# Kernel optimization log

Hardware: AMD Instinct MI355X
Metric: run time of the kernel (lower is better)

The kernel has to match this reference:

```python
import jax, jax.numpy as jnp
import numpy as np

B = 16       # graphs per batch
N = 256      # nodes per graph (Hi-C submatrix bins)
NT = B * N   # total nodes
E = 131072   # total edges
DIN = 32     # input feature dim (HYPERPARAMETERS['input_shape'])
H1, H2 = 16, 32
HID = 32     # ContactCNN hidden dim
W7 = 7       # final conv width


def setup_inputs() -> dict:
    key = jax.random.key(0)
    ks = jax.random.split(key, 16)
    x = jax.random.normal(ks[0], (NT, DIN), dtype=jnp.float32)
    edge_index = jax.random.randint(ks[1], (2, E), 0, NT, dtype=jnp.int64)
    edge_attr = jax.random.uniform(ks[2], (E,), dtype=jnp.float32)
    batch_index = jnp.repeat(jnp.arange(B, dtype=jnp.int64), N)
    s = 0.1
    params = dict(
        W0=jax.random.normal(ks[3], (DIN, H1), dtype=jnp.float32) * s,
        b0=jnp.zeros((H1,), dtype=jnp.float32),
        W1=jax.random.normal(ks[4], (H1, H2), dtype=jnp.float32) * s,
        b1=jnp.zeros((H2,), dtype=jnp.float32),
        W2=jax.random.normal(ks[5], (H2, H2), dtype=jnp.float32) * s,
        b2=jnp.zeros((H2,), dtype=jnp.float32),
        Wc=jax.random.normal(ks[6], (HID, H2), dtype=jnp.float32) * s,  # 1x1 conv: [out=HID, in=H2]
        bc=jnp.zeros((HID,), dtype=jnp.float32),
        Wp=jax.random.normal(ks[7], (1, HID, W7, W7), dtype=jnp.float32) * s,  # OIHW
        bp=jnp.zeros((1,), dtype=jnp.float32),
    )
    return dict(x=x, edge_index=edge_index, edge_attr=edge_attr,
                batch_index=batch_index, **params)


def _gcn_norm(edge_index, edge_weight, n):
    # PyG gcn_norm with improved=True (self-loop fill value 2.0)
    src, dst = edge_index[0], edge_index[1]
    loop = jnp.arange(n, dtype=src.dtype)
    src_a = jnp.concatenate([src, loop])
    dst_a = jnp.concatenate([dst, loop])
    w_a = jnp.concatenate([edge_weight, jnp.full((n,), 2.0, dtype=edge_weight.dtype)])
    deg = jax.ops.segment_sum(w_a, dst_a, num_segments=n)
    deg_safe = jnp.where(deg > 0, deg, 1.0)
    dinv = jnp.where(deg > 0, jax.lax.rsqrt(deg_safe), 0.0)
    norm = dinv[src_a] * w_a * dinv[dst_a]
    return src_a, dst_a, norm


def _gcn_layer(h, W, b, src_a, dst_a, norm, n):
    h = h @ W                                  # [n, out]
    msg = norm[:, None] * h[src_a]             # gather + scale
    return jax.ops.segment_sum(msg, dst_a, num_segments=n) + b  # scatter-add


def reference(x, edge_index, edge_attr, batch_index,
              W0, b0, W1, b1, W2, b2, Wc, bc, Wp, bp):
    n = x.shape[0]
    src_a, dst_a, norm = _gcn_norm(edge_index, edge_attr, n)
    h = jax.nn.relu(_gcn_layer(x, W0, b0, src_a, dst_a, norm, n))
    h = jax.nn.relu(_gcn_layer(h, W1, b1, src_a, dst_a, norm, n))
    h = jax.nn.relu(_gcn_layer(h, W2, b2, src_a, dst_a, norm, n))
    z = h.reshape(B, N, -1)                    # process_graph_batch
    # ContactCNN: broadcast outer product -> 1x1 conv -> ReLU -> 7x7 conv -> sigmoid
    zm = jnp.einsum('bid,bjd->bdij', z, z)     # [B, D, N, N]
    c = jax.nn.relu(jnp.einsum('bdij,hd->bhij', zm, Wc) + bc[None, :, None, None])
    s = jax.lax.conv_general_dilated(
        c, Wp, window_strides=(1, 1), padding='SAME',
        dimension_numbers=('NCHW', 'OIHW', 'NCHW')) + bp[None, :, None, None]
    return jax.nn.sigmoid(s)                   # [B, 1, N, N]
```

## Files before the change

### kernel.cpp

```cpp
#include <hip/hip_runtime.h>
#include <hip/hip_bf16.h>
#include <hip/hip_fp16.h>

#define NT 4096
#define NE 131072

#define OFF_DEG  0
#define OFF_A    16384
#define OFF_G1T  33570816
#define OFF_G2T  33701888
#define OFF_G3T  33964032
#define OFF_H3   34226176
#define OFF_W2T  34488320

typedef __attribute__((ext_vector_type(8))) short bf16x8;
typedef __attribute__((ext_vector_type(4))) float f32x4;

__device__ inline unsigned int align16(unsigned int hi, unsigned int lo) {
#if __has_builtin(__builtin_amdgcn_alignbit)
    return __builtin_amdgcn_alignbit(hi, lo, 16);
#else
    return (lo >> 16) | (hi << 16);
#endif
}

__device__ inline unsigned short bfb(float x) {
    return __hip_bfloat16_raw(__float2bfloat16(x)).x;
}

__device__ inline void atomic_add_bf16(unsigned short* base, unsigned int idx, float v) {
    unsigned long long addr = (unsigned long long)(base + (idx & ~1u));
    unsigned int bits = ((unsigned int)bfb(v)) << ((idx & 1u) * 16);
    asm volatile("global_atomic_pk_add_bf16 %0, %1, off" :: "v"(addr), "v"(bits) : "memory");
}


__global__ __launch_bounds__(256) void k_zerodeg(const int* __restrict__ ei,
                                                 const float* __restrict__ ew,
                                                 float* __restrict__ deg,
                                                 unsigned short* __restrict__ A16) {
    int blk = blockIdx.x, tid = threadIdx.x;
    uint4 z4 = {0u, 0u, 0u, 0u};
    uint4* ap = (uint4*)(A16 + (size_t)blk * 16384);
    #pragma unroll
    for (int k = 0; k < 8; k++) ap[tid + k * 256] = z4;
    int gid = blk * 256 + tid;
    if (gid < NE) atomicAdd(&deg[ei[NE + gid]], ew[gid]);
}

__global__ void k_scatter(const int* __restrict__ ei, const float* __restrict__ ew,
                          const float* __restrict__ deg, unsigned short* __restrict__ A16,
                          const float* __restrict__ x, const float* __restrict__ W0,
                          unsigned short* __restrict__ G1T,
                          const float* __restrict__ Wp, unsigned int* __restrict__ w2) {
    int e = blockIdx.x * 256 + threadIdx.x;
    if (e < NE) {
        int s = ei[e], d = ei[NE + e];
        float v = rsqrtf(deg[s] + 2.f) * ew[e] * rsqrtf(deg[d] + 2.f);
        atomic_add_bf16(A16, (unsigned int)d * 4096u + (unsigned int)s, v);
    }
    if (e < NT) {
        atomic_add_bf16(A16, (unsigned int)e * 4097u, 2.f / (deg[e] + 2.f));
    }
    if (e < NT * 16) {
        int node = e & 4095, co = e >> 12;
        const float4* xr = (const float4*)(x + node * 32);
        float a = 0.f;
        #pragma unroll
        for (int r = 0; r < 8; r++) {
            float4 f = xr[r];
            a += f.x * W0[(r*4+0)*16 + co] + f.y * W0[(r*4+1)*16 + co]
               + f.z * W0[(r*4+2)*16 + co] + f.w * W0[(r*4+3)*16 + co];
        }
        G1T[co * 4096 + node] = bfb(a);
    }
    if (e >= NE - 1568) {
        int k = e - (NE - 1568);
        __half hh = __float2half(Wp[k]);
        __half2 h2 = __halves2half2(hh, hh);
        w2[k] = *(unsigned int*)&h2;
    }
}


template <int NIN, int NOUT, bool LAST>
__global__ __launch_bounds__(512) void k_gcn(const unsigned short* __restrict__ A16,
                                             const unsigned short* __restrict__ Gt,
                                             const float* __restrict__ bias,
                                             const float* __restrict__ W,
                                             unsigned short* __restrict__ Gout) {
    constexpr int T = NIN / 16;
    __shared__ float red[8][T][16][16];
    __shared__ unsigned short wtile[16 * 40];
    int mt = blockIdx.x;
    int tid = threadIdx.x;
    int w = tid >> 6, lane = tid & 63, m = lane & 15, q = lane >> 4;
    int kw = w * 512;

    const unsigned short* arow = A16 + (size_t)(mt * 16 + m) * 4096 + kw + q * 8;
    f32x4 acc[T];
    #pragma unroll
    for (int t = 0; t < T; t++) acc[t] = (f32x4){0.f, 0.f, 0.f, 0.f};

    bf16x8 wfrag;
    if (!LAST && w < NOUT / 16) {
        #pragma unroll
        for (int j = 0; j < 8; j++) {
            int ci = q * 8 + j;
            wfrag[j] = (ci < NIN) ? (short)bfb(W[ci * NOUT + w * 16 + m]) : (short)0;
        }
    }

    #pragma unroll 4
    for (int s = 0; s < 16; s++) {
        bf16x8 bA = *(const bf16x8*)(arow + s * 32);
        #pragma unroll
        for (int t = 0; t < T; t++) {
            bf16x8 af = *(const bf16x8*)(Gt + (size_t)(t * 16 + m) * 4096 + kw + q * 8 + s * 32);
            acc[t] = __builtin_amdgcn_mfma_f32_16x16x32_bf16(af, bA, acc[t], 0, 0, 0);
        }
    }
    #pragma unroll
    for (int t = 0; t < T; t++)
        #pragma unroll
        for (int r = 0; r < 4; r++) red[w][t][q*4 + r][m] = acc[t][r];
    __syncthreads();

    if (tid < T * 256) {
        int dstp = tid & 15, cop = (tid >> 4) & 15, t = tid >> 8;
        float sum = 0.f;
        #pragma unroll
        for (int w8 = 0; w8 < 8; w8++) sum += red[w8][t][cop][dstp];
        int co = t * 16 + cop;
        float val = fmaxf(sum + bias[co], 0.f);
        if (LAST) Gout[(size_t)(mt * 16 + dstp) * 32 + co] = bfb(val);
        else      wtile[dstp * 40 + co] = bfb(val);
    }
    if (!LAST && NIN == 16 && tid >= 256 && tid < 512) {
        int idx = tid - 256;
        wtile[(idx & 15) * 40 + 16 + ((idx >> 4) & 15)] = 0;
    }
    __syncthreads();

    if (!LAST && w < NOUT / 16) {
        bf16x8 af = *(const bf16x8*)&wtile[m * 40 + q * 8];
        f32x4 o = (f32x4){0.f, 0.f, 0.f, 0.f};
        o = __builtin_amdgcn_mfma_f32_16x16x32_bf16(af, wfrag, o, 0, 0, 0);
        uint2 ov;
        ov.x = (unsigned int)bfb(o[0]) | ((unsigned int)bfb(o[1]) << 16);
        ov.y = (unsigned int)bfb(o[2]) | ((unsigned int)bfb(o[3]) << 16);
        *(uint2*)&Gout[(size_t)(w * 16 + m) * 4096 + mt * 16 + q * 4] = ov;
    }
}


__global__ __launch_bounds__(512, 4) void k_cc(const unsigned short* __restrict__ h3,
                                               const float* __restrict__ Wc,
                                               const float* __restrict__ bc,
                                               const unsigned int* __restrict__ w2,
                                               const float* __restrict__ bp,
                                               float* __restrict__ out) {
    __shared__ unsigned short zs[256 * 40];
    __shared__ float wcs[32 * 36];
    __shared__ __align__(16) unsigned short ct[2 * 16 * 272];
    __shared__ __align__(16) unsigned short pt[2][2048];

    int band = blockIdx.x, bb = blockIdx.y;
    int i0 = band * 8;
    int tid = threadIdx.x;
    int lane = tid & 63, w = tid >> 6;
    int m = lane & 15, q = lane >> 4;

    {
        int row = tid >> 1, half = tid & 1;
        const uint4* src = (const uint4*)(h3 + (size_t)(bb * 256 + row) * 32) + half * 2;
        uint4 v0 = src[0], v1 = src[1];
        uint4* dst = (uint4*)&zs[row * 40 + half * 16];
        dst[0] = v0; dst[1] = v1;
    }
    #pragma unroll
    for (int k = tid; k < 1024; k += 512) wcs[(k >> 5) * 36 + (k & 31)] = Wc[k];
    for (int k = tid; k < 2 * 16 * 136; k += 512) ((unsigned int*)ct)[k] = 0;
    __syncthreads();

    bf16x8 bt;
    bool wok;
    {
        int r = i0 - 3 + m;
        wok = (unsigned)r < 256u;
        r = r < 0 ? 0 : (r > 255 ? 255 : r);
        bt = *(const bf16x8*)&zs[r * 40 + q * 8];
    }
    float zaf[2][8];
    #pragma unroll
    for (int jt2 = 0; jt2 < 2; jt2++) {
        bf16x8 za = *(const bf16x8*)&zs[((w * 2 + jt2) * 16 + m) * 40 + q * 8];
        #pragma unroll
        for (int e = 0; e < 8; e++)
            zaf[jt2][e] = __uint_as_float(((unsigned int)(unsigned short)za[e]) << 16);
    }

    int gg = tid >> 8, idx = tid & 255;
    int tx = idx & 31, ty = idx >> 5;
    __half2 acc[4];
    __half2 zh = __float2half2_rn(0.f);
    #pragma unroll
    for (int p = 0; p < 4; p++) acc[p] = zh;

    for (int it = 0; it < 16; it++) {
        #pragma unroll
        for (int g = 0; g < 2; g++) {
            int h = it * 2 + g;
            float wf[8];
            *(float4*)&wf[0] = *(const float4*)&wcs[h * 36 + q * 8];
            *(float4*)&wf[4] = *(const float4*)&wcs[h * 36 + q * 8 + 4];
            float bch = bc[h];
            #pragma unroll
            for (int jt2 = 0; jt2 < 2; jt2++) {
                bf16x8 afv;
                #pragma unroll
                for (int e = 0; e < 8; e++) afv[e] = (short)bfb(zaf[jt2][e] * wf[e]);
                int pos = 4 + (w * 2 + jt2) * 16 + q * 4;
                f32x4 d = (f32x4){0.f, 0.f, 0.f, 0.f};
                d = __builtin_amdgcn_mfma_f32_16x16x32_bf16(afv, bt, d, 0, 0, 0);
                if (wok) {
                    float v0 = fmaxf(d[0] + bch, 0.f);
                    float v1 = fmaxf(d[1] + bch, 0.f);
                    float v2 = fmaxf(d[2] + bch, 0.f);
                    float v3 = fmaxf(d[3] + bch, 0.f);
                    __half2 h0 = __floats2half2_rn(v0, v1);
                    __half2 h1 = __floats2half2_rn(v2, v3);
                    uint2 o2;
                    o2.x = *(unsigned int*)&h0;
                    o2.y = *(unsigned int*)&h1;
                    *(uint2*)&ct[g * 4352 + m * 272 + pos] = o2;
                }
            }
        }
        __syncthreads();

        {
            const unsigned short* C = ct + gg * 4352;
            const __half2* wrow = (const __half2*)w2 + (it * 2 + gg) * 49;
            #pragma unroll
            for (int dr = 0; dr < 7; dr++) {
                const uint4* p4 = (const uint4*)&C[(ty + dr) * 272 + tx * 8];
                uint4 ua = p4[0], ub = p4[1];
                unsigned int E[8] = {ua.x, ua.y, ua.z, ua.w, ub.x, ub.y, ub.z, ub.w};
                unsigned int O[7];
                #pragma unroll
                for (int k = 0; k < 7; k++) O[k] = align16(E[k + 1], E[k]);
                #pragma unroll
                for (int dj = 0; dj < 7; dj++) {
                    __half2 wv = wrow[dr * 7 + dj];
                    #pragma unroll
                    for (int pr = 0; pr < 4; pr++) {
                        int s = 2 * pr + dj + 1;
                        unsigned int pv = (s & 1) ? O[s >> 1] : E[s >> 1];
                        acc[pr] = __hfma2(wv, *(__half2*)&pv, acc[pr]);
                    }
                }
            }
        }
        __syncthreads();
    }

    {
        uint4 v;
        v.x = *(unsigned int*)&acc[0];
        v.y = *(unsigned int*)&acc[1];
        v.z = *(unsigned int*)&acc[2];
        v.w = *(unsigned int*)&acc[3];
        *(uint4*)&pt[gg][ty * 256 + tx * 8] = v;
    }
    __syncthreads();

    {
        int base = tid * 4;
        float fs[4];
        #pragma unroll
        for (int e = 0; e < 4; e++) fs[e] = 0.f;
        #pragma unroll
        for (int g = 0; g < 2; g++) {
            uint2 v = *(const uint2*)&pt[g][base];
            unsigned int uu[2] = {v.x, v.y};
            #pragma unroll
            for (int d = 0; d < 2; d++) {
                float2 f = __half22float2(*(__half2*)&uu[d]);
                fs[2 * d] += f.x; fs[2 * d + 1] += f.y;
            }
        }
        float bpv = bp[0];
        float4 r;
        r.x = 1.0f / (1.0f + __expf(-(fs[0] + bpv)));
        r.y = 1.0f / (1.0f + __expf(-(fs[1] + bpv)));
        r.z = 1.0f / (1.0f + __expf(-(fs[2] + bpv)));
        r.w = 1.0f / (1.0f + __expf(-(fs[3] + bpv)));
        int row = base >> 8, col = base & 255;
        *(float4*)&out[((size_t)(bb * 256) + i0 + row) * 256 + col] = r;
    }
}


extern "C" void kernel_launch(void* const* d_in, const int* in_sizes, int n_in,
                              void* d_out, int out_size, void* d_ws, size_t ws_size,
                              hipStream_t stream) {
    const float* x  = (const float*)d_in[0];
    const int*   ei = (const int*)d_in[1];
    const float* ew = (const float*)d_in[2];
    const float* W0 = (const float*)d_in[4];
    const float* b0 = (const float*)d_in[5];
    const float* W1 = (const float*)d_in[6];
    const float* b1 = (const float*)d_in[7];
    const float* W2 = (const float*)d_in[8];
    const float* b2 = (const float*)d_in[9];
    const float* Wc = (const float*)d_in[10];
    const float* bc = (const float*)d_in[11];
    const float* Wp = (const float*)d_in[12];
    const float* bp = (const float*)d_in[13];

    char* ws = (char*)d_ws;
    float*          deg  = (float*)(ws + OFF_DEG);
    unsigned short* A16  = (unsigned short*)(ws + OFF_A);
    unsigned short* G1T  = (unsigned short*)(ws + OFF_G1T);
    unsigned short* G2T  = (unsigned short*)(ws + OFF_G2T);
    unsigned short* G3T  = (unsigned short*)(ws + OFF_G3T);
    unsigned short* H3   = (unsigned short*)(ws + OFF_H3);
    unsigned int*   w2t  = (unsigned int*)(ws + OFF_W2T);

    (void)hipMemsetAsync(deg, 0, 16384, stream);

    k_zerodeg<<<1024, 256, 0, stream>>>(ei, ew, deg, A16);
    k_scatter<<<NE/256, 256, 0, stream>>>(ei, ew, deg, A16, x, W0, G1T, Wp, w2t);

    k_gcn<16, 32, false><<<256, 512, 0, stream>>>(A16, G1T, b0, W1, G2T);
    k_gcn<32, 32, false><<<256, 512, 0, stream>>>(A16, G2T, b1, W2, G3T);
    k_gcn<32, 32, true> <<<256, 512, 0, stream>>>(A16, G3T, b2, nullptr, H3);

    k_cc<<<dim3(32, 16), 512, 0, stream>>>(H3, Wc, bc, w2t, bp, (float*)d_out);
}
```

Before: 206.6 us.

## Enlarge contact-CNN row bands to 16 and prefetch adjacency fragments in GCN

The contact kernel now computes 16 output rows per block instead of 8, so each block produces a 22-row halo tile with two MFMA column tiles. This halves the redundant halo recomputation and removes the cross-group half-precision reduction through shared memory, since each thread now accumulates both channel groups itself. The 7x7 stencil loads are batched ahead of the FMAs. Separately, the GCN kernel preloads all 16 adjacency fragments into registers before the MFMA loop. In exchange, register pressure rises in both kernels, and the contact grid halves to 256 blocks, which may lower occupancy and parallelism.

```diff
diff --git a/kernel.cpp b/kernel.cpp
--- a/kernel.cpp
+++ b/kernel.cpp
@@ -98,6 +98,11 @@
     int kw = w * 512;
 
     const unsigned short* arow = A16 + (size_t)(mt * 16 + m) * 4096 + kw + q * 8;
+
+    bf16x8 bA[16];
+    #pragma unroll
+    for (int s = 0; s < 16; s++) bA[s] = *(const bf16x8*)(arow + s * 32);
+
     f32x4 acc[T];
     #pragma unroll
     for (int t = 0; t < T; t++) acc[t] = (f32x4){0.f, 0.f, 0.f, 0.f};
@@ -111,13 +116,13 @@
         }
     }
 
-    #pragma unroll 4
+    const unsigned short* gbase = Gt + kw + q * 8 + (size_t)m * 4096;
+    #pragma unroll
     for (int s = 0; s < 16; s++) {
-        bf16x8 bA = *(const bf16x8*)(arow + s * 32);
         #pragma unroll
         for (int t = 0; t < T; t++) {
-            bf16x8 af = *(const bf16x8*)(Gt + (size_t)(t * 16 + m) * 4096 + kw + q * 8 + s * 32);
-            acc[t] = __builtin_amdgcn_mfma_f32_16x16x32_bf16(af, bA, acc[t], 0, 0, 0);
+            bf16x8 af = *(const bf16x8*)(gbase + (size_t)t * 16 * 4096 + s * 32);
+            acc[t] = __builtin_amdgcn_mfma_f32_16x16x32_bf16(af, bA[s], acc[t], 0, 0, 0);
         }
     }
     #pragma unroll
@@ -154,22 +159,22 @@
 }
 
 
-__global__ __launch_bounds__(512, 4) void k_cc(const unsigned short* __restrict__ h3,
-                                               const float* __restrict__ Wc,
-                                               const float* __restrict__ bc,
-                                               const unsigned int* __restrict__ w2,
-                                               const float* __restrict__ bp,
-                                               float* __restrict__ out) {
-    __shared__ unsigned short zs[256 * 40];
+__global__ __launch_bounds__(512) void k_cc(const unsigned short* __restrict__ h3,
+                                            const float* __restrict__ Wc,
+                                            const float* __restrict__ bc,
+                                            const unsigned int* __restrict__ w2,
+                                            const float* __restrict__ bp,
+                                            float* __restrict__ out) {
+    __shared__ __align__(16) unsigned short pool[2 * 32 * 280];
     __shared__ float wcs[32 * 36];
-    __shared__ __align__(16) unsigned short ct[2 * 16 * 272];
-    __shared__ __align__(16) unsigned short pt[2][2048];
 
     int band = blockIdx.x, bb = blockIdx.y;
-    int i0 = band * 8;
+    int i0 = band * 16;
     int tid = threadIdx.x;
     int lane = tid & 63, w = tid >> 6;
     int m = lane & 15, q = lane >> 4;
+
+    unsigned short* zs = pool;
 
     {
         int row = tid >> 1, half = tid & 1;
@@ -180,16 +185,16 @@
     }
     #pragma unroll
     for (int k = tid; k < 1024; k += 512) wcs[(k >> 5) * 36 + (k & 31)] = Wc[k];
-    for (int k = tid; k < 2 * 16 * 136; k += 512) ((unsigned int*)ct)[k] = 0;
-    __syncthreads();
-
-    bf16x8 bt;
-    bool wok;
-    {
-        int r = i0 - 3 + m;
-        wok = (unsigned)r < 256u;
+    __syncthreads();
+
+    bf16x8 bt[2];
+    bool wok[2];
+    #pragma unroll
+    for (int nt = 0; nt < 2; nt++) {
+        int r = i0 - 3 + nt * 16 + m;
+        wok[nt] = (unsigned)r < 256u;
         r = r < 0 ? 0 : (r > 255 ? 255 : r);
-        bt = *(const bf16x8*)&zs[r * 40 + q * 8];
+        bt[nt] = *(const bf16x8*)&zs[r * 40 + q * 8];
     }
     float zaf[2][8];
     #pragma unroll
@@ -199,13 +204,16 @@
         for (int e = 0; e < 8; e++)
             zaf[jt2][e] = __uint_as_float(((unsigned int)(unsigned short)za[e]) << 16);
     }
-
-    int gg = tid >> 8, idx = tid & 255;
-    int tx = idx & 31, ty = idx >> 5;
+    __syncthreads();
+
+    for (int k = tid; k < 8960; k += 512) ((unsigned int*)pool)[k] = 0;
+
+    int tx = tid & 31, ty = tid >> 5;
     __half2 acc[4];
     __half2 zh = __float2half2_rn(0.f);
     #pragma unroll
     for (int p = 0; p < 4; p++) acc[p] = zh;
+    __syncthreads();
 
     for (int it = 0; it < 16; it++) {
         #pragma unroll
@@ -221,32 +229,42 @@
                 #pragma unroll
                 for (int e = 0; e < 8; e++) afv[e] = (short)bfb(zaf[jt2][e] * wf[e]);
                 int pos = 4 + (w * 2 + jt2) * 16 + q * 4;
-                f32x4 d = (f32x4){0.f, 0.f, 0.f, 0.f};
-                d = __builtin_amdgcn_mfma_f32_16x16x32_bf16(afv, bt, d, 0, 0, 0);
-                if (wok) {
-                    float v0 = fmaxf(d[0] + bch, 0.f);
-                    float v1 = fmaxf(d[1] + bch, 0.f);
-                    float v2 = fmaxf(d[2] + bch, 0.f);
-                    float v3 = fmaxf(d[3] + bch, 0.f);
-                    __half2 h0 = __floats2half2_rn(v0, v1);
-                    __half2 h1 = __floats2half2_rn(v2, v3);
-                    uint2 o2;
-                    o2.x = *(unsigned int*)&h0;
-                    o2.y = *(unsigned int*)&h1;
-                    *(uint2*)&ct[g * 4352 + m * 272 + pos] = o2;
+                #pragma unroll
+                for (int nt = 0; nt < 2; nt++) {
+                    f32x4 d = (f32x4){0.f, 0.f, 0.f, 0.f};
+                    d = __builtin_amdgcn_mfma_f32_16x16x32_bf16(afv, bt[nt], d, 0, 0, 0);
+                    if (wok[nt]) {
+                        float v0 = fmaxf(d[0] + bch, 0.f);
+                        float v1 = fmaxf(d[1] + bch, 0.f);
+                        float v2 = fmaxf(d[2] + bch, 0.f);
+                        float v3 = fmaxf(d[3] + bch, 0.f);
+                        __half2 h0 = __floats2half2_rn(v0, v1);
+                        __half2 h1 = __floats2half2_rn(v2, v3);
+                        uint2 o2;
+                        o2.x = *(unsigned int*)&h0;
+                        o2.y = *(unsigned int*)&h1;
+                        *(uint2*)&pool[g * 8960 + (nt * 16 + m) * 280 + pos] = o2;
+                    }
                 }
             }
         }
         __syncthreads();
 
-        {
-            const unsigned short* C = ct + gg * 4352;
-            const __half2* wrow = (const __half2*)w2 + (it * 2 + gg) * 49;
+        #pragma unroll
+        for (int g = 0; g < 2; g++) {
+            const unsigned short* C = pool + g * 8960;
+            const __half2* wrow = (const __half2*)w2 + (it * 2 + g) * 49;
+            uint4 ra[7], rb[7];
             #pragma unroll
             for (int dr = 0; dr < 7; dr++) {
-                const uint4* p4 = (const uint4*)&C[(ty + dr) * 272 + tx * 8];
-                uint4 ua = p4[0], ub = p4[1];
-                unsigned int E[8] = {ua.x, ua.y, ua.z, ua.w, ub.x, ub.y, ub.z, ub.w};
+                const uint4* p4 = (const uint4*)&C[(ty + dr) * 280 + tx * 8];
+                ra[dr] = p4[0];
+                rb[dr] = p4[1];
+            }
+            #pragma unroll
+            for (int dr = 0; dr < 7; dr++) {
+                unsigned int E[8] = {ra[dr].x, ra[dr].y, ra[dr].z, ra[dr].w,
+                                     rb[dr].x, rb[dr].y, rb[dr].z, rb[dr].w};
                 unsigned int O[7];
                 #pragma unroll
                 for (int k = 0; k < 7; k++) O[k] = align16(E[k + 1], E[k]);
@@ -266,38 +284,19 @@
     }
 
     {
-        uint4 v;
-        v.x = *(unsigned int*)&acc[0];
-        v.y = *(unsigned int*)&acc[1];
-        v.z = *(unsigned int*)&acc[2];
-        v.w = *(unsigned int*)&acc[3];
-        *(uint4*)&pt[gg][ty * 256 + tx * 8] = v;
-    }
-    __syncthreads();
-
-    {
-        int base = tid * 4;
-        float fs[4];
-        #pragma unroll
-        for (int e = 0; e < 4; e++) fs[e] = 0.f;
-        #pragma unroll
-        for (int g = 0; g < 2; g++) {
-            uint2 v = *(const uint2*)&pt[g][base];
-            unsigned int uu[2] = {v.x, v.y};
-            #pragma unroll
-            for (int d = 0; d < 2; d++) {
-                float2 f = __half22float2(*(__half2*)&uu[d]);
-                fs[2 * d] += f.x; fs[2 * d + 1] += f.y;
-            }
-        }
         float bpv = bp[0];
-        float4 r;
-        r.x = 1.0f / (1.0f + __expf(-(fs[0] + bpv)));
-        r.y = 1.0f / (1.0f + __expf(-(fs[1] + bpv)));
-        r.z = 1.0f / (1.0f + __expf(-(fs[2] + bpv)));
-        r.w = 1.0f / (1.0f + __expf(-(fs[3] + bpv)));
-        int row = base >> 8, col = base & 255;
-        *(float4*)&out[((size_t)(bb * 256) + i0 + row) * 256 + col] = r;
+        float fs[8];
+        #pragma unroll
+        for (int pr = 0; pr < 4; pr++) {
+            float2 f = __half22float2(acc[pr]);
+            fs[2 * pr] = f.x; fs[2 * pr + 1] = f.y;
+        }
+        float rs[8];
+        #pragma unroll
+        for (int e = 0; e < 8; e++) rs[e] = 1.0f / (1.0f + __expf(-(fs[e] + bpv)));
+        float* op = &out[((size_t)(bb * 256) + i0 + ty) * 256 + tx * 8];
+        *(float4*)op = make_float4(rs[0], rs[1], rs[2], rs[3]);
+        *(float4*)(op + 4) = make_float4(rs[4], rs[5], rs[6], rs[7]);
     }
 }
 
@@ -337,5 +336,5 @@
     k_gcn<32, 32, false><<<256, 512, 0, stream>>>(A16, G2T, b1, W2, G3T);
     k_gcn<32, 32, true> <<<256, 512, 0, stream>>>(A16, G3T, b2, nullptr, H3);
 
-    k_cc<<<dim3(32, 16), 512, 0, stream>>>(H3, Wc, bc, w2t, bp, (float*)d_out);
-}
+    k_cc<<<dim3(16, 16), 512, 0, stream>>>(H3, Wc, bc, w2t, bp, (float*)d_out);
+}
```

Result: no change. 210.4 us (+1.9%).

## Preload GCN A-row fragments and restructure 7x7 conv for row reuse across four channels

Applied to the files above, without the earlier changes.

In the GCN kernel, all sixteen A-row bf16 fragments are loaded into registers up front and the k-loop is fully unrolled, so loads can be issued early ahead of the MFMAs. In the contact kernel, the shared buffers are merged into one reused pool. Each iteration now stages four 1x1-conv channels instead of two, and each thread computes two output rows, so every loaded input row feeds both outputs (8 row loads instead of 14). This is meant to cut LDS traffic and halve the number of barrier-separated iterations, at the cost of higher register pressure and a larger staging footprint that may lower occupancy.

```diff
diff --git a/kernel.cpp b/kernel.cpp
--- a/kernel.cpp
+++ b/kernel.cpp
@@ -98,6 +98,11 @@
     int kw = w * 512;
 
     const unsigned short* arow = A16 + (size_t)(mt * 16 + m) * 4096 + kw + q * 8;
+
+    bf16x8 bA[16];
+    #pragma unroll
+    for (int s = 0; s < 16; s++) bA[s] = *(const bf16x8*)(arow + s * 32);
+
     f32x4 acc[T];
     #pragma unroll
     for (int t = 0; t < T; t++) acc[t] = (f32x4){0.f, 0.f, 0.f, 0.f};
@@ -111,13 +116,13 @@
         }
     }
 
-    #pragma unroll 4
+    const unsigned short* gbase = Gt + kw + q * 8 + (size_t)m * 4096;
+    #pragma unroll
     for (int s = 0; s < 16; s++) {
-        bf16x8 bA = *(const bf16x8*)(arow + s * 32);
         #pragma unroll
         for (int t = 0; t < T; t++) {
-            bf16x8 af = *(const bf16x8*)(Gt + (size_t)(t * 16 + m) * 4096 + kw + q * 8 + s * 32);
-            acc[t] = __builtin_amdgcn_mfma_f32_16x16x32_bf16(af, bA, acc[t], 0, 0, 0);
+            bf16x8 af = *(const bf16x8*)(gbase + (size_t)t * 16 * 4096 + s * 32);
+            acc[t] = __builtin_amdgcn_mfma_f32_16x16x32_bf16(af, bA[s], acc[t], 0, 0, 0);
         }
     }
     #pragma unroll
@@ -160,10 +165,8 @@
                                                const unsigned int* __restrict__ w2,
                                                const float* __restrict__ bp,
                                                float* __restrict__ out) {
-    __shared__ unsigned short zs[256 * 40];
+    __shared__ __align__(16) unsigned short pool[15680];
     __shared__ float wcs[32 * 36];
-    __shared__ __align__(16) unsigned short ct[2 * 16 * 272];
-    __shared__ __align__(16) unsigned short pt[2][2048];
 
     int band = blockIdx.x, bb = blockIdx.y;
     int i0 = band * 8;
@@ -175,42 +178,47 @@
         int row = tid >> 1, half = tid & 1;
         const uint4* src = (const uint4*)(h3 + (size_t)(bb * 256 + row) * 32) + half * 2;
         uint4 v0 = src[0], v1 = src[1];
-        uint4* dst = (uint4*)&zs[row * 40 + half * 16];
+        uint4* dst = (uint4*)&pool[row * 40 + half * 16];
         dst[0] = v0; dst[1] = v1;
     }
     #pragma unroll
     for (int k = tid; k < 1024; k += 512) wcs[(k >> 5) * 36 + (k & 31)] = Wc[k];
-    for (int k = tid; k < 2 * 16 * 136; k += 512) ((unsigned int*)ct)[k] = 0;
     __syncthreads();
 
     bf16x8 bt;
     bool wok;
     {
         int r = i0 - 3 + m;
-        wok = (unsigned)r < 256u;
-        r = r < 0 ? 0 : (r > 255 ? 255 : r);
-        bt = *(const bf16x8*)&zs[r * 40 + q * 8];
+        wok = ((unsigned)r < 256u) && (m < 14);
+        int rc = r < 0 ? 0 : (r > 255 ? 255 : r);
+        bt = *(const bf16x8*)&pool[rc * 40 + q * 8];
     }
     float zaf[2][8];
     #pragma unroll
     for (int jt2 = 0; jt2 < 2; jt2++) {
-        bf16x8 za = *(const bf16x8*)&zs[((w * 2 + jt2) * 16 + m) * 40 + q * 8];
+        bf16x8 za = *(const bf16x8*)&pool[((w * 2 + jt2) * 16 + m) * 40 + q * 8];
         #pragma unroll
         for (int e = 0; e < 8; e++)
             zaf[jt2][e] = __uint_as_float(((unsigned int)(unsigned short)za[e]) << 16);
     }
-
-    int gg = tid >> 8, idx = tid & 255;
+    __syncthreads();
+
+    for (int k = tid; k < 7840; k += 512) ((unsigned int*)pool)[k] = 0;
+    __syncthreads();
+
+    int gg = tid >> 7, idx = tid & 127;
     int tx = idx & 31, ty = idx >> 5;
-    __half2 acc[4];
+    __half2 acc[2][4];
     __half2 zh = __float2half2_rn(0.f);
     #pragma unroll
-    for (int p = 0; p < 4; p++) acc[p] = zh;
-
-    for (int it = 0; it < 16; it++) {
-        #pragma unroll
-        for (int g = 0; g < 2; g++) {
-            int h = it * 2 + g;
+    for (int o = 0; o < 2; o++)
+        #pragma unroll
+        for (int p = 0; p < 4; p++) acc[o][p] = zh;
+
+    for (int it = 0; it < 8; it++) {
+        #pragma unroll
+        for (int g = 0; g < 4; g++) {
+            int h = it * 4 + g;
             float wf[8];
             *(float4*)&wf[0] = *(const float4*)&wcs[h * 36 + q * 8];
             *(float4*)&wf[4] = *(const float4*)&wcs[h * 36 + q * 8 + 4];
@@ -233,31 +241,36 @@
                     uint2 o2;
                     o2.x = *(unsigned int*)&h0;
                     o2.y = *(unsigned int*)&h1;
-                    *(uint2*)&ct[g * 4352 + m * 272 + pos] = o2;
+                    *(uint2*)&pool[g * 3920 + m * 280 + pos] = o2;
                 }
             }
         }
         __syncthreads();
 
         {
-            const unsigned short* C = ct + gg * 4352;
-            const __half2* wrow = (const __half2*)w2 + (it * 2 + gg) * 49;
+            const unsigned short* C = pool + gg * 3920;
+            const __half2* wrow = (const __half2*)w2 + (it * 4 + gg) * 49;
             #pragma unroll
-            for (int dr = 0; dr < 7; dr++) {
-                const uint4* p4 = (const uint4*)&C[(ty + dr) * 272 + tx * 8];
+            for (int dr = 0; dr < 8; dr++) {
+                const uint4* p4 = (const uint4*)&C[(ty * 2 + dr) * 280 + tx * 8];
                 uint4 ua = p4[0], ub = p4[1];
                 unsigned int E[8] = {ua.x, ua.y, ua.z, ua.w, ub.x, ub.y, ub.z, ub.w};
                 unsigned int O[7];
                 #pragma unroll
                 for (int k = 0; k < 7; k++) O[k] = align16(E[k + 1], E[k]);
                 #pragma unroll
-                for (int dj = 0; dj < 7; dj++) {
-                    __half2 wv = wrow[dr * 7 + dj];
+                for (int o = 0; o < 2; o++) {
+                    if (dr - o < 0 || dr - o > 6) continue;
+                    int di = dr - o;
                     #pragma unroll
-                    for (int pr = 0; pr < 4; pr++) {
-                        int s = 2 * pr + dj + 1;
-                        unsigned int pv = (s & 1) ? O[s >> 1] : E[s >> 1];
-                        acc[pr] = __hfma2(wv, *(__half2*)&pv, acc[pr]);
+                    for (int dj = 0; dj < 7; dj++) {
+                        __half2 wv = wrow[di * 7 + dj];
+                        #pragma unroll
+                        for (int pr = 0; pr < 4; pr++) {
+                            int s = 2 * pr + dj + 1;
+                            unsigned int pv = (s & 1) ? O[s >> 1] : E[s >> 1];
+                            acc[o][pr] = __hfma2(wv, *(__half2*)&pv, acc[o][pr]);
+                        }
                     }
                 }
             }
@@ -265,30 +278,26 @@
         __syncthreads();
     }
 
-    {
+    #pragma unroll
+    for (int o = 0; o < 2; o++) {
         uint4 v;
-        v.x = *(unsigned int*)&acc[0];
-        v.y = *(unsigned int*)&acc[1];
-        v.z = *(unsigned int*)&acc[2];
-        v.w = *(unsigned int*)&acc[3];
-        *(uint4*)&pt[gg][ty * 256 + tx * 8] = v;
+        v.x = *(unsigned int*)&acc[o][0];
+        v.y = *(unsigned int*)&acc[o][1];
+        v.z = *(unsigned int*)&acc[o][2];
+        v.w = *(unsigned int*)&acc[o][3];
+        *(uint4*)&pool[gg * 2048 + (ty * 2 + o) * 256 + tx * 8] = v;
     }
     __syncthreads();
 
     {
         int base = tid * 4;
-        float fs[4];
-        #pragma unroll
-        for (int e = 0; e < 4; e++) fs[e] = 0.f;
-        #pragma unroll
-        for (int g = 0; g < 2; g++) {
-            uint2 v = *(const uint2*)&pt[g][base];
-            unsigned int uu[2] = {v.x, v.y};
-            #pragma unroll
-            for (int d = 0; d < 2; d++) {
-                float2 f = __half22float2(*(__half2*)&uu[d]);
-                fs[2 * d] += f.x; fs[2 * d + 1] += f.y;
-            }
+        float fs[4] = {0.f, 0.f, 0.f, 0.f};
+        #pragma unroll
+        for (int g = 0; g < 4; g++) {
+            uint2 v = *(const uint2*)&pool[g * 2048 + base];
+            float2 f0 = __half22float2(*(__half2*)&v.x);
+            float2 f1 = __half22float2(*(__half2*)&v.y);
+            fs[0] += f0.x; fs[1] += f0.y; fs[2] += f1.x; fs[3] += f1.y;
         }
         float bpv = bp[0];
         float4 r;
```

After: 196.3 us. 1.05x faster.
